# Kernel tuning notes

Hardware: AMD Instinct MI355X
Metric: run time of the kernel (lower is better)

The kernel has to match this reference:

```python
import jax, jax.numpy as jnp
import numpy as np


def setup_inputs() -> dict:
    key = jax.random.key(0)
    ks = jax.random.split(key, 12)
    B, T, S, D, A, E, L, V = 32, 64, 64, 1024, 512, 256, 1024, 12000
    s = 0.02  # weight scale for numerical stability
    return {
        "targets": jax.random.randint(ks[0], (B, T), 0, V),
        "options": jax.random.normal(ks[1], (B, S, D), jnp.float32),
        "h0": jax.random.normal(ks[2], (B, L), jnp.float32),
        "c0": jnp.zeros((B, L), jnp.float32),
        "emb": jax.random.normal(ks[3], (V, E), jnp.float32) * s,
        "W1": jax.random.normal(ks[4], (L, A), jnp.float32) * s,
        "b1": jnp.zeros((A,), jnp.float32),
        "W2": jax.random.normal(ks[5], (D, A), jnp.float32) * s,
        "b2": jnp.zeros((A,), jnp.float32),
        "Va": jax.random.normal(ks[6], (A, 1), jnp.float32) * s,
        "bVa": jnp.zeros((1,), jnp.float32),
        "Wx": jax.random.normal(ks[7], (D + E, 4 * L), jnp.float32) * s,
        "Wh": jax.random.normal(ks[8], (L, 4 * L), jnp.float32) * s,
        "bl": jnp.zeros((4 * L,), jnp.float32),
        "Wd": jax.random.normal(ks[9], (L, V), jnp.float32) * s,
        "bd": jnp.zeros((V,), jnp.float32),
    }


def reference(targets, options, h0, c0, emb, W1, b1, W2, b2, Va, bVa,
              Wx, Wh, bl, Wd, bd):
    L = h0.shape[-1]
    # W2(options) is step-invariant: hoist out of recurrent loop. [B,S,A]
    opt_proj = jnp.einsum('bsd,da->bsa', options, W2) + b2

    def step(carry, x_ids):
        h, c = carry
        # Bahdanau attention: score = V(tanh(W1(h) + W2(options)))
        score = jnp.tanh(h @ W1 + b1)[:, None, :] + opt_proj        # [B,S,A]
        score = jnp.einsum('bsa,ao->bso', score, Va) + bVa          # [B,S,1]
        w = jax.nn.softmax(score, axis=1)                           # [B,S,1]
        context = jnp.sum(w * options, axis=1)                      # [B,D]
        x = jnp.concatenate([context, emb[x_ids]], axis=-1)         # [B,D+E]
        # Keras LSTM cell, gate order i, f, g, o
        z = x @ Wx + h @ Wh + bl                                    # [B,4L]
        i, f, g, o = jnp.split(z, 4, axis=-1)
        c = jax.nn.sigmoid(f) * c + jax.nn.sigmoid(i) * jnp.tanh(g)
        h = jax.nn.sigmoid(o) * jnp.tanh(c)
        probs = jax.nn.softmax(h @ Wd + bd, axis=-1)                # [B,V]
        return (h, c), (probs, w[..., 0])

    (h, c), (out, attn) = jax.lax.scan(step, (h0, c0), targets.T)
    output = jnp.transpose(out, (1, 0, 2))   # [B,T,V]
    attention = attn[-1][..., None]          # last-step attention weights [B,S,1]
    return output, h, c, attention
```

## Files before the change

kernel.cpp:

```cpp
#include <hip/hip_runtime.h>
#include <math.h>


typedef __bf16 bf16;
typedef _Float16 fp16;
typedef __attribute__((ext_vector_type(8))) __bf16 bf16x8;
typedef __attribute__((ext_vector_type(8))) _Float16 fp16x8;
typedef __attribute__((ext_vector_type(4))) float f32x4;

constexpr int B = 32, T = 64, S = 64, D = 1024, A = 512, E = 256, L = 1024, V = 12000;
constexpr int G = 4096;
constexpr size_t N_PROBS = (size_t)B * T * V;

__device__ inline void load_lds16(const void* g, void* l) {
  __builtin_amdgcn_global_load_lds(
      (const __attribute__((address_space(1))) unsigned int*)g,
      (__attribute__((address_space(3))) unsigned int*)l, 16, 0, 0);
}


__global__ void k_v2(const float* __restrict__ W2, const float* __restrict__ Va,
                     float* __restrict__ v2) {
  int gw = (blockIdx.x * blockDim.x + threadIdx.x) >> 6;
  int lane = threadIdx.x & 63;
  if (gw >= D) return;
  float acc = 0.f;
  for (int a = lane; a < A; a += 64) acc += W2[(size_t)gw * A + a] * Va[a];
  #pragma unroll
  for (int off = 32; off; off >>= 1) acc += __shfl_down(acc, off);
  if (lane == 0) v2[gw] = acc;
}

__global__ void k_score(const float* __restrict__ options, const float* __restrict__ v2,
                        float* __restrict__ w) {
  int row = (blockIdx.x * blockDim.x + threadIdx.x) >> 6;
  int lane = threadIdx.x & 63;
  if (row >= B * S) return;
  const float* orow = options + (size_t)row * D;
  float acc = 0.f;
  for (int d = lane; d < D; d += 64) acc += orow[d] * v2[d];
  #pragma unroll
  for (int off = 32; off; off >>= 1) acc += __shfl_down(acc, off);
  if (lane == 0) w[row] = acc;
}

__global__ __launch_bounds__(256) void k_attnctx(
    const float* __restrict__ options, const float* __restrict__ wat,
    float* __restrict__ oattn, float* __restrict__ ctx) {
  __shared__ float sw[64];
  const int b = blockIdx.x, tid = threadIdx.x;
  if (tid < 64) {
    float v = wat[b * 64 + tid];
    float m = v;
    #pragma unroll
    for (int off = 32; off; off >>= 1) m = fmaxf(m, __shfl_xor(m, off));
    float e = expf(v - m);
    float s = e;
    #pragma unroll
    for (int off = 32; off; off >>= 1) s += __shfl_xor(s, off);
    float res = e / s;
    sw[tid] = res;
    oattn[b * 64 + tid] = res;
  }
  __syncthreads();
  for (int d = tid; d < D; d += 256) {
    float acc = 0.f;
    #pragma unroll 8
    for (int s = 0; s < 64; ++s)
      acc += sw[s] * options[((size_t)(b * 64 + s)) * D + d];
    ctx[b * D + d] = acc;
  }
}

__global__ __launch_bounds__(256) void k_cx_part(
    const float* __restrict__ ctx, const float* __restrict__ Wx,
    float* __restrict__ cxp) {
  const int jt = blockIdx.x & 15;
  const int bg = (blockIdx.x >> 4) & 3;
  const int kc = blockIdx.x >> 6;
  const int j = jt * 256 + threadIdx.x;
  const int b0 = bg * 8, d0 = kc * 128;
  float acc[8];
  #pragma unroll
  for (int bb = 0; bb < 8; ++bb) acc[bb] = 0.f;
  for (int d = 0; d < 128; ++d) {
    float wv = Wx[(size_t)(d0 + d) * G + j];
    #pragma unroll
    for (int bb = 0; bb < 8; ++bb)
      acc[bb] = fmaf(ctx[(b0 + bb) * D + d0 + d], wv, acc[bb]);
  }
  #pragma unroll
  for (int bb = 0; bb < 8; ++bb)
    cxp[((size_t)kc * 32 + b0 + bb) * G + j] = acc[bb];
}

__global__ void k_cx_reduce(const float* __restrict__ cxp, const float* __restrict__ bl,
                            float* __restrict__ cx) {
  int i = blockIdx.x * 256 + threadIdx.x;
  float s = bl[i & 4095];
  #pragma unroll
  for (int kc = 0; kc < 8; ++kc) s += cxp[(size_t)kc * 131072 + i];
  cx[i] = s;
}


__global__ void k_eg(const int* __restrict__ targets, const float* __restrict__ emb,
                     bf16* __restrict__ eg_hi, bf16* __restrict__ eg_lo) {
  int r = blockIdx.x, e = threadIdx.x;
  int tok = targets[r];
  float x = emb[(size_t)tok * E + e];
  bf16 hi = (bf16)x;
  eg_hi[(size_t)r * E + e] = hi;
  eg_lo[(size_t)r * E + e] = (bf16)(x - (float)hi);
}

__global__ __launch_bounds__(256) void k_wx2t(const float* __restrict__ Wx,
                                              bf16* __restrict__ t_hi,
                                              bf16* __restrict__ t_lo) {
  __shared__ float s[64][65];
  const int et = blockIdx.x >> 6, jt = blockIdx.x & 63;
  const int e0 = et * 64, j0 = jt * 64;
  const int tid = threadIdx.x;
  const int jj = tid & 63;
  #pragma unroll
  for (int k = 0; k < 16; ++k) {
    int ee = k * 4 + (tid >> 6);
    s[ee][jj] = Wx[(size_t)(D + e0 + ee) * G + j0 + jj];
  }
  __syncthreads();
  const int jc = tid >> 2, eq = tid & 3;
  bf16x8 h0, h1, l0, l1;
  #pragma unroll
  for (int i = 0; i < 8; ++i) {
    float a = s[eq * 16 + i][jc], b = s[eq * 16 + 8 + i][jc];
    bf16 ah = (bf16)a, bh = (bf16)b;
    h0[i] = ah; l0[i] = (bf16)(a - (float)ah);
    h1[i] = bh; l1[i] = (bf16)(b - (float)bh);
  }
  size_t dst = (size_t)(j0 + jc) * E + e0 + eq * 16;
  *(bf16x8*)(t_hi + dst) = h0; *(bf16x8*)(t_hi + dst + 8) = h1;
  *(bf16x8*)(t_lo + dst) = l0; *(bf16x8*)(t_lo + dst + 8) = l1;
}

__global__ __launch_bounds__(256) void k_whp(const float* __restrict__ Wh,
                                             fp16* __restrict__ p) {
  __shared__ float s[64][65];
  const int lt = blockIdx.x & 15, ct = blockIdx.x >> 4;
  const int l0 = lt * 64, c0 = ct * 64;
  const int tid = threadIdx.x;
  const int cc = tid & 63;
  #pragma unroll
  for (int k = 0; k < 16; ++k) {
    int ll = k * 4 + (tid >> 6);
    s[ll][cc] = Wh[(size_t)(l0 + ll) * G + c0 + cc];
  }
  __syncthreads();
  const int c = tid >> 2, lq = tid & 3;
  const int col = c0 + c, g = col >> 10, jj = col & 1023;
  const int rowp = ((jj >> 2) << 4) + (g << 2) + (jj & 3);
  fp16x8 o0, o1;
  #pragma unroll
  for (int i = 0; i < 8; ++i) {
    o0[i] = (fp16)s[lq * 16 + i][c];
    o1[i] = (fp16)s[lq * 16 + 8 + i][c];
  }
  size_t dst = (size_t)rowp * L + l0 + lq * 16;
  *(fp16x8*)(p + dst) = o0;
  *(fp16x8*)(p + dst + 8) = o1;
}

__global__ void k_h0split(const float* __restrict__ h0, const float* __restrict__ c0,
                          fp16* __restrict__ h16, float* __restrict__ cst,
                          float* __restrict__ hf32) {
  int i = blockIdx.x * 256 + threadIdx.x;
  float x = h0[i];
  h16[i] = (fp16)x;
  hf32[i] = x;
  cst[i] = c0[i];
}

__global__ __launch_bounds__(256) void k_pre_mfma(
    const bf16* __restrict__ Ah, const bf16* __restrict__ Al,
    const bf16* __restrict__ Bh, const bf16* __restrict__ Bl,
    const float* __restrict__ cx, fp16* __restrict__ pre16) {
  __shared__ __align__(16) char lds[65536];
  char* sAh = lds;
  char* sAl = lds + 16384;
  char* sBh = lds + 32768;
  char* sBl = lds + 49152;
  const int bid = blockIdx.x;
  const int swz = (bid & 7) * 64 + (bid >> 3);
  const int mt = swz >> 5, nt = swz & 31;
  const int m0 = mt * 128, n0 = nt * 128;
  const int tid = threadIdx.x, w = tid >> 6, lane = tid & 63;
  const int wr = w >> 1, wc = w & 1;

  f32x4 acc[4][4];
  #pragma unroll
  for (int i = 0; i < 4; ++i)
    #pragma unroll
    for (int j = 0; j < 4; ++j) acc[i][j] = (f32x4){0.f, 0.f, 0.f, 0.f};

  int rowc[4], sloc[4];
  #pragma unroll
  for (int i = 0; i < 4; ++i) {
    int c = i * 4 + w;
    rowc[i] = c * 8 + (lane >> 3);
    sloc[i] = (lane & 7) ^ (rowc[i] & 7);
  }

  for (int kk = 0; kk < 4; ++kk) {
    if (kk) __syncthreads();
    const char* gah = (const char*)Ah + kk * 128;
    const char* gal = (const char*)Al + kk * 128;
    const char* gbh = (const char*)Bh + kk * 128;
    const char* gbl = (const char*)Bl + kk * 128;
    #pragma unroll
    for (int i = 0; i < 4; ++i) {
      int c = i * 4 + w;
      load_lds16(gah + (size_t)(m0 + rowc[i]) * 512 + sloc[i] * 16, sAh + c * 1024);
      load_lds16(gal + (size_t)(m0 + rowc[i]) * 512 + sloc[i] * 16, sAl + c * 1024);
      load_lds16(gbh + (size_t)(n0 + rowc[i]) * 512 + sloc[i] * 16, sBh + c * 1024);
      load_lds16(gbl + (size_t)(n0 + rowc[i]) * 512 + sloc[i] * 16, sBl + c * 1024);
    }
    __syncthreads();
    #pragma unroll
    for (int ks = 0; ks < 2; ++ks) {
      bf16x8 avh[4], avl[4], bvh[4], bvl[4];
      #pragma unroll
      for (int f = 0; f < 4; ++f) {
        int ra = wr * 64 + f * 16 + (lane & 15);
        int ca = (ks * 4 + (lane >> 4)) ^ (ra & 7);
        avh[f] = *(const bf16x8*)(sAh + ra * 128 + ca * 16);
        avl[f] = *(const bf16x8*)(sAl + ra * 128 + ca * 16);
        int rb = wc * 64 + f * 16 + (lane & 15);
        int cb = (ks * 4 + (lane >> 4)) ^ (rb & 7);
        bvh[f] = *(const bf16x8*)(sBh + rb * 128 + cb * 16);
        bvl[f] = *(const bf16x8*)(sBl + rb * 128 + cb * 16);
      }
      #pragma unroll
      for (int fm = 0; fm < 4; ++fm)
        #pragma unroll
        for (int fn = 0; fn < 4; ++fn) {
          acc[fm][fn] = __builtin_amdgcn_mfma_f32_16x16x32_bf16(avh[fm], bvh[fn], acc[fm][fn], 0, 0, 0);
          acc[fm][fn] = __builtin_amdgcn_mfma_f32_16x16x32_bf16(avh[fm], bvl[fn], acc[fm][fn], 0, 0, 0);
          acc[fm][fn] = __builtin_amdgcn_mfma_f32_16x16x32_bf16(avl[fm], bvh[fn], acc[fm][fn], 0, 0, 0);
        }
    }
  }

  const int r0o = m0 + wr * 64 + ((lane >> 4) << 2);
  const int c0o = n0 + wc * 64 + (lane & 15);
  #pragma unroll
  for (int fn = 0; fn < 4; ++fn) {
    int colg = c0o + fn * 16;
    #pragma unroll
    for (int fm = 0; fm < 4; ++fm) {
      #pragma unroll
      for (int r = 0; r < 4; ++r) {
        int row = r0o + fm * 16 + r;
        float v = acc[fm][fn][r] + cx[(size_t)(row >> 6) * G + colg];
        pre16[(size_t)row * G + colg] = (fp16)v;
      }
    }
  }
}

__global__ __launch_bounds__(512) void k_step4(
    const fp16* __restrict__ Whp, const fp16* __restrict__ pre16,
    const fp16* __restrict__ hin, fp16* __restrict__ hout,
    float* __restrict__ cst, float* __restrict__ hf32,
    fp16* __restrict__ Hb16, int t) {
  __shared__ float zred[8 * 2 * 64 * 4];
  __shared__ float zf[32][16];
  const int jb = blockIdx.x;
  const int tid = threadIdx.x;
  const int w = tid >> 6, lane = tid & 63;
  const int fr = lane & 15, kc = lane >> 4;

  float pf[4];
  float cprev = 0.f;
  const int gb = tid >> 2, gjo = tid & 3, gj = jb * 4 + gjo;
  if (tid < 128) {
    const size_t pbase = (size_t)(gb * 64 + t) * G + gj;
    #pragma unroll
    for (int g = 0; g < 4; ++g) pf[g] = (float)pre16[pbase + g * 1024];
    cprev = cst[gb * 1024 + gj];
  }

  f32x4 acc[2];
  acc[0] = (f32x4){0.f, 0.f, 0.f, 0.f};
  acc[1] = (f32x4){0.f, 0.f, 0.f, 0.f};
  const fp16* bb = Whp + (size_t)(jb * 16 + fr) * L;
  #pragma unroll
  for (int kk = 0; kk < 4; ++kk) {
    const int k0 = (w * 4 + kk) * 32 + kc * 8;
    fp16x8 bv = *(const fp16x8*)(bb + k0);
    #pragma unroll
    for (int m = 0; m < 2; ++m) {
      fp16x8 av = *(const fp16x8*)(hin + (size_t)(m * 16 + fr) * L + k0);
      acc[m] = __builtin_amdgcn_mfma_f32_16x16x32_f16(av, bv, acc[m], 0, 0, 0);
    }
  }
  #pragma unroll
  for (int m = 0; m < 2; ++m)
    *(f32x4*)&zred[((w * 2 + m) * 64 + lane) * 4] = acc[m];
  __syncthreads();
  {
    const int b = tid >> 4, c = tid & 15;
    const int lane2 = (((b & 15) >> 2) << 4) | c;
    const int reg = b & 3, m = b >> 4;
    float s = 0.f;
    #pragma unroll
    for (int ww = 0; ww < 8; ++ww)
      s += zred[((ww * 2 + m) * 64 + lane2) * 4 + reg];
    zf[b][c] = s;
  }
  __syncthreads();
  if (tid < 128) {
    float zi = zf[gb][gjo] + pf[0];
    float zff = zf[gb][4 + gjo] + pf[1];
    float zg = zf[gb][8 + gjo] + pf[2];
    float zo = zf[gb][12 + gjo] + pf[3];
    float si = 1.f / (1.f + expf(-zi));
    float sf = 1.f / (1.f + expf(-zff));
    float tg = tanhf(zg);
    float so = 1.f / (1.f + expf(-zo));
    float cn = sf * cprev + si * tg;
    float hn = so * tanhf(cn);
    const int hi_idx = gb * 1024 + gj;
    cst[hi_idx] = cn;
    hout[hi_idx] = (fp16)hn;
    hf32[hi_idx] = hn;
    Hb16[(size_t)(gb * 64 + t) * L + gj] = (fp16)hn;
  }
}

__global__ __launch_bounds__(256) void k_wdt(const float* __restrict__ Wd,
                                             fp16* __restrict__ Wdt) {
  __shared__ float s[64][65];
  const int lt = blockIdx.x & 15;
  const int vt = blockIdx.x >> 4;
  const int l0 = lt * 64, v0 = vt * 64;
  const int tid = threadIdx.x;
  const int lv = tid & 63;
  #pragma unroll
  for (int k = 0; k < 16; ++k) {
    int ll = k * 4 + (tid >> 6);
    int v = v0 + lv;
    s[ll][lv] = (v < V) ? Wd[(size_t)(l0 + ll) * V + v] : 0.f;
  }
  __syncthreads();
  const int vv = tid >> 2, lq = tid & 3;
  fp16x8 o0, o1;
  #pragma unroll
  for (int j = 0; j < 8; ++j) {
    o0[j] = (fp16)s[lq * 16 + j][vv];
    o1[j] = (fp16)s[lq * 16 + 8 + j][vv];
  }
  fp16* dst = Wdt + (size_t)(v0 + vv) * 1024 + l0 + lq * 16;
  *(fp16x8*)dst = o0;
  *(fp16x8*)(dst + 8) = o1;
}

__global__ __launch_bounds__(256) void k_logits_mfma(
    const fp16* __restrict__ Ag, const fp16* __restrict__ Btg,
    const float* __restrict__ bd, float* __restrict__ out) {
  __shared__ __align__(16) char lds[65536];
  char* sA = lds;
  char* sB = lds + 16384;
  const int bid = blockIdx.x;
  const int wg = (bid & 7) * 188 + (bid >> 3);
  const int mt = wg / 94, nt = wg % 94;
  const int m0 = mt * 128, n0 = nt * 128;
  const int tid = threadIdx.x, w = tid >> 6, lane = tid & 63;
  const int wr = w >> 1, wc = w & 1;

  f32x4 acc[4][4];
  #pragma unroll
  for (int i = 0; i < 4; ++i)
    #pragma unroll
    for (int j = 0; j < 4; ++j) acc[i][j] = (f32x4){0.f, 0.f, 0.f, 0.f};

  int rowc[4], sloc[4];
  #pragma unroll
  for (int i = 0; i < 4; ++i) {
    int c = i * 4 + w;
    rowc[i] = c * 8 + (lane >> 3);
    sloc[i] = (lane & 7) ^ (rowc[i] & 7);
  }

  for (int kk = 0; kk < 16; ++kk) {
    if (kk) __syncthreads();
    const char* ga = (const char*)Ag + kk * 128;
    const char* gb = (const char*)Btg + kk * 128;
    #pragma unroll
    for (int i = 0; i < 4; ++i) {
      int c = i * 4 + w;
      load_lds16(ga + (size_t)(m0 + rowc[i]) * 2048 + sloc[i] * 16, sA + c * 1024);
      load_lds16(gb + (size_t)(n0 + rowc[i]) * 2048 + sloc[i] * 16, sB + c * 1024);
    }
    __syncthreads();
    #pragma unroll
    for (int ks = 0; ks < 2; ++ks) {
      fp16x8 av[4], bv[4];
      #pragma unroll
      for (int f = 0; f < 4; ++f) {
        int ra = wr * 64 + f * 16 + (lane & 15);
        int ca = (ks * 4 + (lane >> 4)) ^ (ra & 7);
        av[f] = *(const fp16x8*)(sA + ra * 128 + ca * 16);
        int rb = wc * 64 + f * 16 + (lane & 15);
        int cb = (ks * 4 + (lane >> 4)) ^ (rb & 7);
        bv[f] = *(const fp16x8*)(sB + rb * 128 + cb * 16);
      }
      #pragma unroll
      for (int fm = 0; fm < 4; ++fm)
        #pragma unroll
        for (int fn = 0; fn < 4; ++fn)
          acc[fm][fn] = __builtin_amdgcn_mfma_f32_16x16x32_f16(
              av[fm], bv[fn], acc[fm][fn], 0, 0, 0);
    }
  }

  __syncthreads();
  float* ctile = (float*)lds;
  const int c0o = n0 + wc * 64 + (lane & 15);
  #pragma unroll
  for (int fn = 0; fn < 4; ++fn) {
    int colg = c0o + fn * 16;
    float bv = (colg < V) ? bd[colg] : 0.f;
    int col = wc * 64 + fn * 16 + (lane & 15);
    #pragma unroll
    for (int fm = 0; fm < 4; ++fm) {
      int row = wr * 64 + fm * 16 + ((lane >> 4) << 2);
      #pragma unroll
      for (int r = 0; r < 4; ++r)
        ctile[(row + r) * 128 + col] = acc[fm][fn][r] + bv;
    }
  }
  __syncthreads();
  #pragma unroll
  for (int it = 0; it < 16; ++it) {
    int idx = it * 256 + tid;
    int row = idx >> 5, ch = idx & 31;
    int colg = n0 + ch * 4;
    if (colg < V)
      *(float4*)&out[(size_t)(m0 + row) * V + colg] = *(float4*)&ctile[row * 128 + ch * 4];
  }
}

__global__ __launch_bounds__(256) void k_softmax(float* __restrict__ logits) {
  __shared__ float srow[V];
  __shared__ float sred[4];
  float* row = logits + (size_t)blockIdx.x * V;
  const int tid = threadIdx.x;
  const float4* rv = (const float4*)row;
  float4* sv = (float4*)srow;
  float m = -3.4e38f;
  for (int i = tid; i < 3000; i += 256) {
    float4 x = rv[i];
    sv[i] = x;
    m = fmaxf(fmaxf(m, fmaxf(x.x, x.y)), fmaxf(x.z, x.w));
  }
  #pragma unroll
  for (int off = 32; off; off >>= 1) m = fmaxf(m, __shfl_xor(m, off));
  if ((tid & 63) == 0) sred[tid >> 6] = m;
  __syncthreads();
  const float M = fmaxf(fmaxf(sred[0], sred[1]), fmaxf(sred[2], sred[3]));
  float s = 0.f;
  for (int i = tid; i < 3000; i += 256) {
    float4 x = sv[i];
    x.x = __expf(x.x - M); x.y = __expf(x.y - M);
    x.z = __expf(x.z - M); x.w = __expf(x.w - M);
    sv[i] = x;
    s += x.x + x.y + x.z + x.w;
  }
  #pragma unroll
  for (int off = 32; off; off >>= 1) s += __shfl_xor(s, off);
  __syncthreads();
  if ((tid & 63) == 0) sred[tid >> 6] = s;
  __syncthreads();
  const float inv = 1.f / (sred[0] + sred[1] + sred[2] + sred[3]);
  float4* ov = (float4*)row;
  for (int i = tid; i < 3000; i += 256) {
    float4 x = sv[i];
    x.x *= inv; x.y *= inv; x.z *= inv; x.w *= inv;
    ov[i] = x;
  }
}

__global__ void k_finalize(const float* __restrict__ hf32, const float* __restrict__ cst,
                           float* __restrict__ oh, float* __restrict__ oc) {
  int i = blockIdx.x * 256 + threadIdx.x;
  if (i < B * L) {
    oh[i] = hf32[i];
    oc[i] = cst[i];
  }
}


extern "C" void kernel_launch(void* const* d_in, const int* in_sizes, int n_in,
                              void* d_out, int out_size, void* d_ws, size_t ws_size,
                              hipStream_t stream) {
  const int*   targets = (const int*)d_in[0];
  const float* options = (const float*)d_in[1];
  const float* h0      = (const float*)d_in[2];
  const float* c0      = (const float*)d_in[3];
  const float* emb     = (const float*)d_in[4];
  const float* W2      = (const float*)d_in[7];
  const float* Va      = (const float*)d_in[9];
  const float* Wx      = (const float*)d_in[11];
  const float* Wh      = (const float*)d_in[12];
  const float* bl      = (const float*)d_in[13];
  const float* Wd      = (const float*)d_in[14];
  const float* bd      = (const float*)d_in[15];

  float* out      = (float*)d_out;
  float* out_h    = out + N_PROBS;
  float* out_c    = out_h + (size_t)B * L;
  float* out_attn = out_c + (size_t)B * L;

  char* wsb = (char*)d_ws;
  float* v2     = (float*)(wsb);
  float* wat    = (float*)(wsb + 4096);
  float* ctx    = (float*)(wsb + 12288);
  float* cx     = (float*)(wsb + 143360);
  float* cst    = (float*)(wsb + 667648);
  fp16*  hA     = (fp16*)(wsb + 798720);
  fp16*  hB     = (fp16*)(wsb + 864256);
  float* hf32   = (float*)(wsb + 929792);
  bf16*  Eg_hi  = (bf16*)(wsb + 1191936);
  bf16*  Eg_lo  = (bf16*)(wsb + 2240512);
  bf16*  Wx2t_hi= (bf16*)(wsb + 3289088);
  bf16*  Wx2t_lo= (bf16*)(wsb + 5386240);
  fp16*  Hb16   = (fp16*)(wsb + 1191936);
  fp16*  Whp    = (fp16*)(wsb + 7483392);
  fp16*  pre16  = (fp16*)(wsb + 15872000);
  float* cxp    = (float*)(wsb + 15872000);
  fp16*  Wdt    = (fp16*)(wsb + 7483392);

  k_v2<<<256, 256, 0, stream>>>(W2, Va, v2);
  k_score<<<512, 256, 0, stream>>>(options, v2, wat);
  k_attnctx<<<32, 256, 0, stream>>>(options, wat, out_attn, ctx);
  k_cx_part<<<512, 256, 0, stream>>>(ctx, Wx, cxp);
  k_cx_reduce<<<512, 256, 0, stream>>>(cxp, bl, cx);

  k_eg<<<2048, 256, 0, stream>>>(targets, emb, Eg_hi, Eg_lo);
  k_wx2t<<<256, 256, 0, stream>>>(Wx, Wx2t_hi, Wx2t_lo);
  k_whp<<<1024, 256, 0, stream>>>(Wh, Whp);

  k_pre_mfma<<<512, 256, 0, stream>>>(Eg_hi, Eg_lo, Wx2t_hi, Wx2t_lo, cx, pre16);
  k_h0split<<<128, 256, 0, stream>>>(h0, c0, hA, cst, hf32);

  for (int t = 0; t < T; ++t) {
    const fp16* hin = (t & 1) ? hB : hA;
    fp16* hout = (t & 1) ? hA : hB;
    k_step4<<<256, 512, 0, stream>>>(Whp, pre16, hin, hout, cst, hf32, Hb16, t);
  }

  k_wdt<<<188 * 16, 256, 0, stream>>>(Wd, Wdt);
  k_logits_mfma<<<1504, 256, 0, stream>>>(Hb16, Wdt, bd, out);
  k_softmax<<<B * T, 256, 0, stream>>>(out);
  k_finalize<<<128, 256, 0, stream>>>(hf32, cst, out_h, out_c);
}
```

Before: 586.1 us.

## Use single fp16 GEMM for embedding projection and pack pre-activations per step

The bf16 hi/lo split of the embedding and Wx slices is replaced by plain fp16, so the pre-activation GEMM loads half the data and issues one MFMA per tile instead of three. Its output is written in a per-timestep, per-block layout, letting each recurrent step fetch its four gate values with one vector load instead of four strided loads. The logits GEMM tile order is also changed so consecutive blocks share M tiles along N. The cost is lower precision in the input projection.

```diff
diff --git a/kernel.cpp b/kernel.cpp
--- a/kernel.cpp
+++ b/kernel.cpp
@@ -6,6 +6,7 @@
 typedef _Float16 fp16;
 typedef __attribute__((ext_vector_type(8))) __bf16 bf16x8;
 typedef __attribute__((ext_vector_type(8))) _Float16 fp16x8;
+typedef __attribute__((ext_vector_type(4))) _Float16 fp16x4;
 typedef __attribute__((ext_vector_type(4))) float f32x4;
 
 constexpr int B = 32, T = 64, S = 64, D = 1024, A = 512, E = 256, L = 1024, V = 12000;
@@ -105,18 +106,14 @@
 
 
 __global__ void k_eg(const int* __restrict__ targets, const float* __restrict__ emb,
-                     bf16* __restrict__ eg_hi, bf16* __restrict__ eg_lo) {
+                     fp16* __restrict__ eg) {
   int r = blockIdx.x, e = threadIdx.x;
   int tok = targets[r];
-  float x = emb[(size_t)tok * E + e];
-  bf16 hi = (bf16)x;
-  eg_hi[(size_t)r * E + e] = hi;
-  eg_lo[(size_t)r * E + e] = (bf16)(x - (float)hi);
+  eg[(size_t)r * E + e] = (fp16)emb[(size_t)tok * E + e];
 }
 
 __global__ __launch_bounds__(256) void k_wx2t(const float* __restrict__ Wx,
-                                              bf16* __restrict__ t_hi,
-                                              bf16* __restrict__ t_lo) {
+                                              fp16* __restrict__ t16) {
   __shared__ float s[64][65];
   const int et = blockIdx.x >> 6, jt = blockIdx.x & 63;
   const int e0 = et * 64, j0 = jt * 64;
@@ -129,17 +126,15 @@
   }
   __syncthreads();
   const int jc = tid >> 2, eq = tid & 3;
-  bf16x8 h0, h1, l0, l1;
+  fp16x8 o0, o1;
   #pragma unroll
   for (int i = 0; i < 8; ++i) {
-    float a = s[eq * 16 + i][jc], b = s[eq * 16 + 8 + i][jc];
-    bf16 ah = (bf16)a, bh = (bf16)b;
-    h0[i] = ah; l0[i] = (bf16)(a - (float)ah);
-    h1[i] = bh; l1[i] = (bf16)(b - (float)bh);
+    o0[i] = (fp16)s[eq * 16 + i][jc];
+    o1[i] = (fp16)s[eq * 16 + 8 + i][jc];
   }
   size_t dst = (size_t)(j0 + jc) * E + e0 + eq * 16;
-  *(bf16x8*)(t_hi + dst) = h0; *(bf16x8*)(t_hi + dst + 8) = h1;
-  *(bf16x8*)(t_lo + dst) = l0; *(bf16x8*)(t_lo + dst + 8) = l1;
+  *(fp16x8*)(t16 + dst) = o0;
+  *(fp16x8*)(t16 + dst + 8) = o1;
 }
 
 __global__ __launch_bounds__(256) void k_whp(const float* __restrict__ Wh,
@@ -180,14 +175,11 @@
 }
 
 __global__ __launch_bounds__(256) void k_pre_mfma(
-    const bf16* __restrict__ Ah, const bf16* __restrict__ Al,
-    const bf16* __restrict__ Bh, const bf16* __restrict__ Bl,
-    const float* __restrict__ cx, fp16* __restrict__ pre16) {
-  __shared__ __align__(16) char lds[65536];
-  char* sAh = lds;
-  char* sAl = lds + 16384;
-  char* sBh = lds + 32768;
-  char* sBl = lds + 49152;
+    const fp16* __restrict__ Ag, const fp16* __restrict__ Bg,
+    const float* __restrict__ cx, fp16* __restrict__ prep) {
+  __shared__ __align__(16) char lds[32768];
+  char* sA = lds;
+  char* sB = lds + 16384;
   const int bid = blockIdx.x;
   const int swz = (bid & 7) * 64 + (bid >> 3);
   const int mt = swz >> 5, nt = swz & 31;
@@ -211,194 +203,13 @@
 
   for (int kk = 0; kk < 4; ++kk) {
     if (kk) __syncthreads();
-    const char* gah = (const char*)Ah + kk * 128;
-    const char* gal = (const char*)Al + kk * 128;
-    const char* gbh = (const char*)Bh + kk * 128;
-    const char* gbl = (const char*)Bl + kk * 128;
+    const char* ga = (const char*)Ag + kk * 128;
+    const char* gb = (const char*)Bg + kk * 128;
     #pragma unroll
     for (int i = 0; i < 4; ++i) {
       int c = i * 4 + w;
-      load_lds16(gah + (size_t)(m0 + rowc[i]) * 512 + sloc[i] * 16, sAh + c * 1024);
-      load_lds16(gal + (size_t)(m0 + rowc[i]) * 512 + sloc[i] * 16, sAl + c * 1024);
-      load_lds16(gbh + (size_t)(n0 + rowc[i]) * 512 + sloc[i] * 16, sBh + c * 1024);
-      load_lds16(gbl + (size_t)(n0 + rowc[i]) * 512 + sloc[i] * 16, sBl + c * 1024);
-    }
-    __syncthreads();
-    #pragma unroll
-    for (int ks = 0; ks < 2; ++ks) {
-      bf16x8 avh[4], avl[4], bvh[4], bvl[4];
-      #pragma unroll
-      for (int f = 0; f < 4; ++f) {
-        int ra = wr * 64 + f * 16 + (lane & 15);
-        int ca = (ks * 4 + (lane >> 4)) ^ (ra & 7);
-        avh[f] = *(const bf16x8*)(sAh + ra * 128 + ca * 16);
-        avl[f] = *(const bf16x8*)(sAl + ra * 128 + ca * 16);
-        int rb = wc * 64 + f * 16 + (lane & 15);
-        int cb = (ks * 4 + (lane >> 4)) ^ (rb & 7);
-        bvh[f] = *(const bf16x8*)(sBh + rb * 128 + cb * 16);
-        bvl[f] = *(const bf16x8*)(sBl + rb * 128 + cb * 16);
-      }
-      #pragma unroll
-      for (int fm = 0; fm < 4; ++fm)
-        #pragma unroll
-        for (int fn = 0; fn < 4; ++fn) {
-          acc[fm][fn] = __builtin_amdgcn_mfma_f32_16x16x32_bf16(avh[fm], bvh[fn], acc[fm][fn], 0, 0, 0);
-          acc[fm][fn] = __builtin_amdgcn_mfma_f32_16x16x32_bf16(avh[fm], bvl[fn], acc[fm][fn], 0, 0, 0);
-          acc[fm][fn] = __builtin_amdgcn_mfma_f32_16x16x32_bf16(avl[fm], bvh[fn], acc[fm][fn], 0, 0, 0);
-        }
-    }
-  }
-
-  const int r0o = m0 + wr * 64 + ((lane >> 4) << 2);
-  const int c0o = n0 + wc * 64 + (lane & 15);
-  #pragma unroll
-  for (int fn = 0; fn < 4; ++fn) {
-    int colg = c0o + fn * 16;
-    #pragma unroll
-    for (int fm = 0; fm < 4; ++fm) {
-      #pragma unroll
-      for (int r = 0; r < 4; ++r) {
-        int row = r0o + fm * 16 + r;
-        float v = acc[fm][fn][r] + cx[(size_t)(row >> 6) * G + colg];
-        pre16[(size_t)row * G + colg] = (fp16)v;
-      }
-    }
-  }
-}
-
-__global__ __launch_bounds__(512) void k_step4(
-    const fp16* __restrict__ Whp, const fp16* __restrict__ pre16,
-    const fp16* __restrict__ hin, fp16* __restrict__ hout,
-    float* __restrict__ cst, float* __restrict__ hf32,
-    fp16* __restrict__ Hb16, int t) {
-  __shared__ float zred[8 * 2 * 64 * 4];
-  __shared__ float zf[32][16];
-  const int jb = blockIdx.x;
-  const int tid = threadIdx.x;
-  const int w = tid >> 6, lane = tid & 63;
-  const int fr = lane & 15, kc = lane >> 4;
-
-  float pf[4];
-  float cprev = 0.f;
-  const int gb = tid >> 2, gjo = tid & 3, gj = jb * 4 + gjo;
-  if (tid < 128) {
-    const size_t pbase = (size_t)(gb * 64 + t) * G + gj;
-    #pragma unroll
-    for (int g = 0; g < 4; ++g) pf[g] = (float)pre16[pbase + g * 1024];
-    cprev = cst[gb * 1024 + gj];
-  }
-
-  f32x4 acc[2];
-  acc[0] = (f32x4){0.f, 0.f, 0.f, 0.f};
-  acc[1] = (f32x4){0.f, 0.f, 0.f, 0.f};
-  const fp16* bb = Whp + (size_t)(jb * 16 + fr) * L;
-  #pragma unroll
-  for (int kk = 0; kk < 4; ++kk) {
-    const int k0 = (w * 4 + kk) * 32 + kc * 8;
-    fp16x8 bv = *(const fp16x8*)(bb + k0);
-    #pragma unroll
-    for (int m = 0; m < 2; ++m) {
-      fp16x8 av = *(const fp16x8*)(hin + (size_t)(m * 16 + fr) * L + k0);
-      acc[m] = __builtin_amdgcn_mfma_f32_16x16x32_f16(av, bv, acc[m], 0, 0, 0);
-    }
-  }
-  #pragma unroll
-  for (int m = 0; m < 2; ++m)
-    *(f32x4*)&zred[((w * 2 + m) * 64 + lane) * 4] = acc[m];
-  __syncthreads();
-  {
-    const int b = tid >> 4, c = tid & 15;
-    const int lane2 = (((b & 15) >> 2) << 4) | c;
-    const int reg = b & 3, m = b >> 4;
-    float s = 0.f;
-    #pragma unroll
-    for (int ww = 0; ww < 8; ++ww)
-      s += zred[((ww * 2 + m) * 64 + lane2) * 4 + reg];
-    zf[b][c] = s;
-  }
-  __syncthreads();
-  if (tid < 128) {
-    float zi = zf[gb][gjo] + pf[0];
-    float zff = zf[gb][4 + gjo] + pf[1];
-    float zg = zf[gb][8 + gjo] + pf[2];
-    float zo = zf[gb][12 + gjo] + pf[3];
-    float si = 1.f / (1.f + expf(-zi));
-    float sf = 1.f / (1.f + expf(-zff));
-    float tg = tanhf(zg);
-    float so = 1.f / (1.f + expf(-zo));
-    float cn = sf * cprev + si * tg;
-    float hn = so * tanhf(cn);
-    const int hi_idx = gb * 1024 + gj;
-    cst[hi_idx] = cn;
-    hout[hi_idx] = (fp16)hn;
-    hf32[hi_idx] = hn;
-    Hb16[(size_t)(gb * 64 + t) * L + gj] = (fp16)hn;
-  }
-}
-
-__global__ __launch_bounds__(256) void k_wdt(const float* __restrict__ Wd,
-                                             fp16* __restrict__ Wdt) {
-  __shared__ float s[64][65];
-  const int lt = blockIdx.x & 15;
-  const int vt = blockIdx.x >> 4;
-  const int l0 = lt * 64, v0 = vt * 64;
-  const int tid = threadIdx.x;
-  const int lv = tid & 63;
-  #pragma unroll
-  for (int k = 0; k < 16; ++k) {
-    int ll = k * 4 + (tid >> 6);
-    int v = v0 + lv;
-    s[ll][lv] = (v < V) ? Wd[(size_t)(l0 + ll) * V + v] : 0.f;
-  }
-  __syncthreads();
-  const int vv = tid >> 2, lq = tid & 3;
-  fp16x8 o0, o1;
-  #pragma unroll
-  for (int j = 0; j < 8; ++j) {
-    o0[j] = (fp16)s[lq * 16 + j][vv];
-    o1[j] = (fp16)s[lq * 16 + 8 + j][vv];
-  }
-  fp16* dst = Wdt + (size_t)(v0 + vv) * 1024 + l0 + lq * 16;
-  *(fp16x8*)dst = o0;
-  *(fp16x8*)(dst + 8) = o1;
-}
-
-__global__ __launch_bounds__(256) void k_logits_mfma(
-    const fp16* __restrict__ Ag, const fp16* __restrict__ Btg,
-    const float* __restrict__ bd, float* __restrict__ out) {
-  __shared__ __align__(16) char lds[65536];
-  char* sA = lds;
-  char* sB = lds + 16384;
-  const int bid = blockIdx.x;
-  const int wg = (bid & 7) * 188 + (bid >> 3);
-  const int mt = wg / 94, nt = wg % 94;
-  const int m0 = mt * 128, n0 = nt * 128;
-  const int tid = threadIdx.x, w = tid >> 6, lane = tid & 63;
-  const int wr = w >> 1, wc = w & 1;
-
-  f32x4 acc[4][4];
-  #pragma unroll
-  for (int i = 0; i < 4; ++i)
-    #pragma unroll
-    for (int j = 0; j < 4; ++j) acc[i][j] = (f32x4){0.f, 0.f, 0.f, 0.f};
-
-  int rowc[4], sloc[4];
-  #pragma unroll
-  for (int i = 0; i < 4; ++i) {
-    int c = i * 4 + w;
-    rowc[i] = c * 8 + (lane >> 3);
-    sloc[i] = (lane & 7) ^ (rowc[i] & 7);
-  }
-
-  for (int kk = 0; kk < 16; ++kk) {
-    if (kk) __syncthreads();
-    const char* ga = (const char*)Ag + kk * 128;
-    const char* gb = (const char*)Btg + kk * 128;
-    #pragma unroll
-    for (int i = 0; i < 4; ++i) {
-      int c = i * 4 + w;
-      load_lds16(ga + (size_t)(m0 + rowc[i]) * 2048 + sloc[i] * 16, sA + c * 1024);
-      load_lds16(gb + (size_t)(n0 + rowc[i]) * 2048 + sloc[i] * 16, sB + c * 1024);
+      load_lds16(ga + (size_t)(m0 + rowc[i]) * 512 + sloc[i] * 16, sA + c * 1024);
+      load_lds16(gb + (size_t)(n0 + rowc[i]) * 512 + sloc[i] * 16, sB + c * 1024);
     }
     __syncthreads();
     #pragma unroll
@@ -422,6 +233,182 @@
     }
   }
 
+  const int r0o = m0 + wr * 64 + ((lane >> 4) << 2);
+  const int c0o = n0 + wc * 64 + (lane & 15);
+  #pragma unroll
+  for (int fn = 0; fn < 4; ++fn) {
+    int colg = c0o + fn * 16;
+    int g = colg >> 10, jj = colg & 1023;
+    int jb = jj >> 2, jo = jj & 3;
+    #pragma unroll
+    for (int fm = 0; fm < 4; ++fm) {
+      #pragma unroll
+      for (int r = 0; r < 4; ++r) {
+        int row = r0o + fm * 16 + r;
+        int b = row >> 6, t = row & 63;
+        float v = acc[fm][fn][r] + cx[(size_t)b * G + colg];
+        prep[(((size_t)t * 256 + jb) * 32 + b) * 16 + jo * 4 + g] = (fp16)v;
+      }
+    }
+  }
+}
+
+__global__ __launch_bounds__(512) void k_step4(
+    const fp16* __restrict__ Whp, const fp16* __restrict__ prep,
+    const fp16* __restrict__ hin, fp16* __restrict__ hout,
+    float* __restrict__ cst, float* __restrict__ hf32,
+    fp16* __restrict__ Hb16, int t) {
+  __shared__ float zred[8 * 2 * 64 * 4];
+  __shared__ float zf[32][16];
+  const int jb = blockIdx.x;
+  const int tid = threadIdx.x;
+  const int w = tid >> 6, lane = tid & 63;
+  const int fr = lane & 15, kc = lane >> 4;
+
+  float pf[4];
+  float cprev = 0.f;
+  const int gb = tid >> 2, gjo = tid & 3, gj = jb * 4 + gjo;
+  if (tid < 128) {
+    fp16x4 pv = *(const fp16x4*)(prep + (((size_t)t * 256 + jb) * 32 + gb) * 16 + gjo * 4);
+    #pragma unroll
+    for (int g = 0; g < 4; ++g) pf[g] = (float)pv[g];
+    cprev = cst[gb * 1024 + gj];
+  }
+
+  f32x4 acc[2];
+  acc[0] = (f32x4){0.f, 0.f, 0.f, 0.f};
+  acc[1] = (f32x4){0.f, 0.f, 0.f, 0.f};
+  const fp16* bb = Whp + (size_t)(jb * 16 + fr) * L;
+  #pragma unroll
+  for (int kk = 0; kk < 4; ++kk) {
+    const int k0 = (w * 4 + kk) * 32 + kc * 8;
+    fp16x8 bv = *(const fp16x8*)(bb + k0);
+    #pragma unroll
+    for (int m = 0; m < 2; ++m) {
+      fp16x8 av = *(const fp16x8*)(hin + (size_t)(m * 16 + fr) * L + k0);
+      acc[m] = __builtin_amdgcn_mfma_f32_16x16x32_f16(av, bv, acc[m], 0, 0, 0);
+    }
+  }
+  #pragma unroll
+  for (int m = 0; m < 2; ++m)
+    *(f32x4*)&zred[((w * 2 + m) * 64 + lane) * 4] = acc[m];
+  __syncthreads();
+  {
+    const int b = tid >> 4, c = tid & 15;
+    const int lane2 = (((b & 15) >> 2) << 4) | c;
+    const int reg = b & 3, m = b >> 4;
+    float s = 0.f;
+    #pragma unroll
+    for (int ww = 0; ww < 8; ++ww)
+      s += zred[((ww * 2 + m) * 64 + lane2) * 4 + reg];
+    zf[b][c] = s;
+  }
+  __syncthreads();
+  if (tid < 128) {
+    float zi = zf[gb][gjo] + pf[0];
+    float zff = zf[gb][4 + gjo] + pf[1];
+    float zg = zf[gb][8 + gjo] + pf[2];
+    float zo = zf[gb][12 + gjo] + pf[3];
+    float si = 1.f / (1.f + expf(-zi));
+    float sf = 1.f / (1.f + expf(-zff));
+    float tg = tanhf(zg);
+    float so = 1.f / (1.f + expf(-zo));
+    float cn = sf * cprev + si * tg;
+    float hn = so * tanhf(cn);
+    const int hi_idx = gb * 1024 + gj;
+    cst[hi_idx] = cn;
+    hout[hi_idx] = (fp16)hn;
+    hf32[hi_idx] = hn;
+    Hb16[(size_t)(gb * 64 + t) * L + gj] = (fp16)hn;
+  }
+}
+
+__global__ __launch_bounds__(256) void k_wdt(const float* __restrict__ Wd,
+                                             fp16* __restrict__ Wdt) {
+  __shared__ float s[64][65];
+  const int lt = blockIdx.x & 15;
+  const int vt = blockIdx.x >> 4;
+  const int l0 = lt * 64, v0 = vt * 64;
+  const int tid = threadIdx.x;
+  const int lv = tid & 63;
+  #pragma unroll
+  for (int k = 0; k < 16; ++k) {
+    int ll = k * 4 + (tid >> 6);
+    int v = v0 + lv;
+    s[ll][lv] = (v < V) ? Wd[(size_t)(l0 + ll) * V + v] : 0.f;
+  }
+  __syncthreads();
+  const int vv = tid >> 2, lq = tid & 3;
+  fp16x8 o0, o1;
+  #pragma unroll
+  for (int j = 0; j < 8; ++j) {
+    o0[j] = (fp16)s[lq * 16 + j][vv];
+    o1[j] = (fp16)s[lq * 16 + 8 + j][vv];
+  }
+  fp16* dst = Wdt + (size_t)(v0 + vv) * 1024 + l0 + lq * 16;
+  *(fp16x8*)dst = o0;
+  *(fp16x8*)(dst + 8) = o1;
+}
+
+__global__ __launch_bounds__(256) void k_logits_mfma(
+    const fp16* __restrict__ Ag, const fp16* __restrict__ Btg,
+    const float* __restrict__ bd, float* __restrict__ out) {
+  __shared__ __align__(16) char lds[65536];
+  char* sA = lds;
+  char* sB = lds + 16384;
+  const int bid = blockIdx.x;
+  const int wg = (bid & 7) * 188 + (bid >> 3);
+  const int nt = wg >> 4, mt = wg & 15;
+  const int m0 = mt * 128, n0 = nt * 128;
+  const int tid = threadIdx.x, w = tid >> 6, lane = tid & 63;
+  const int wr = w >> 1, wc = w & 1;
+
+  f32x4 acc[4][4];
+  #pragma unroll
+  for (int i = 0; i < 4; ++i)
+    #pragma unroll
+    for (int j = 0; j < 4; ++j) acc[i][j] = (f32x4){0.f, 0.f, 0.f, 0.f};
+
+  int rowc[4], sloc[4];
+  #pragma unroll
+  for (int i = 0; i < 4; ++i) {
+    int c = i * 4 + w;
+    rowc[i] = c * 8 + (lane >> 3);
+    sloc[i] = (lane & 7) ^ (rowc[i] & 7);
+  }
+
+  for (int kk = 0; kk < 16; ++kk) {
+    if (kk) __syncthreads();
+    const char* ga = (const char*)Ag + kk * 128;
+    const char* gb = (const char*)Btg + kk * 128;
+    #pragma unroll
+    for (int i = 0; i < 4; ++i) {
+      int c = i * 4 + w;
+      load_lds16(ga + (size_t)(m0 + rowc[i]) * 2048 + sloc[i] * 16, sA + c * 1024);
+      load_lds16(gb + (size_t)(n0 + rowc[i]) * 2048 + sloc[i] * 16, sB + c * 1024);
+    }
+    __syncthreads();
+    #pragma unroll
+    for (int ks = 0; ks < 2; ++ks) {
+      fp16x8 av[4], bv[4];
+      #pragma unroll
+      for (int f = 0; f < 4; ++f) {
+        int ra = wr * 64 + f * 16 + (lane & 15);
+        int ca = (ks * 4 + (lane >> 4)) ^ (ra & 7);
+        av[f] = *(const fp16x8*)(sA + ra * 128 + ca * 16);
+        int rb = wc * 64 + f * 16 + (lane & 15);
+        int cb = (ks * 4 + (lane >> 4)) ^ (rb & 7);
+        bv[f] = *(const fp16x8*)(sB + rb * 128 + cb * 16);
+      }
+      #pragma unroll
+      for (int fm = 0; fm < 4; ++fm)
+        #pragma unroll
+        for (int fn = 0; fn < 4; ++fn)
+          acc[fm][fn] = __builtin_amdgcn_mfma_f32_16x16x32_f16(
+              av[fm], bv[fn], acc[fm][fn], 0, 0, 0);
+    }
+  }
+
   __syncthreads();
   float* ctile = (float*)lds;
   const int c0o = n0 + wc * 64 + (lane & 15);
@@ -529,13 +516,11 @@
   fp16*  hA     = (fp16*)(wsb + 798720);
   fp16*  hB     = (fp16*)(wsb + 864256);
   float* hf32   = (float*)(wsb + 929792);
-  bf16*  Eg_hi  = (bf16*)(wsb + 1191936);
-  bf16*  Eg_lo  = (bf16*)(wsb + 2240512);
-  bf16*  Wx2t_hi= (bf16*)(wsb + 3289088);
-  bf16*  Wx2t_lo= (bf16*)(wsb + 5386240);
+  fp16*  Eg16   = (fp16*)(wsb + 1191936);
+  fp16*  Wx2t16 = (fp16*)(wsb + 2240512);
   fp16*  Hb16   = (fp16*)(wsb + 1191936);
   fp16*  Whp    = (fp16*)(wsb + 7483392);
-  fp16*  pre16  = (fp16*)(wsb + 15872000);
+  fp16*  prep   = (fp16*)(wsb + 15872000);
   float* cxp    = (float*)(wsb + 15872000);
   fp16*  Wdt    = (fp16*)(wsb + 7483392);
 
@@ -545,17 +530,17 @@
   k_cx_part<<<512, 256, 0, stream>>>(ctx, Wx, cxp);
   k_cx_reduce<<<512, 256, 0, stream>>>(cxp, bl, cx);
 
-  k_eg<<<2048, 256, 0, stream>>>(targets, emb, Eg_hi, Eg_lo);
-  k_wx2t<<<256, 256, 0, stream>>>(Wx, Wx2t_hi, Wx2t_lo);
+  k_eg<<<2048, 256, 0, stream>>>(targets, emb, Eg16);
+  k_wx2t<<<256, 256, 0, stream>>>(Wx, Wx2t16);
   k_whp<<<1024, 256, 0, stream>>>(Wh, Whp);
 
-  k_pre_mfma<<<512, 256, 0, stream>>>(Eg_hi, Eg_lo, Wx2t_hi, Wx2t_lo, cx, pre16);
+  k_pre_mfma<<<512, 256, 0, stream>>>(Eg16, Wx2t16, cx, prep);
   k_h0split<<<128, 256, 0, stream>>>(h0, c0, hA, cst, hf32);
 
   for (int t = 0; t < T; ++t) {
     const fp16* hin = (t & 1) ? hB : hA;
     fp16* hout = (t & 1) ? hA : hB;
-    k_step4<<<256, 512, 0, stream>>>(Whp, pre16, hin, hout, cst, hf32, Hb16, t);
+    k_step4<<<256, 512, 0, stream>>>(Whp, prep, hin, hout, cst, hf32, Hb16, t);
   }
 
   k_wdt<<<188 * 16, 256, 0, stream>>>(Wd, Wdt);
```

New measurement: 560.4 us. 1.05x faster.
